# Kernel tuning notes

Measured on AMD Instinct MI355X. Metric: run time of the kernel, lower is better.

## Reference

```python
import jax, jax.numpy as jnp
import numpy as np

N_FEATURES = 16
N_FREQUENCIES = 256
TIME_AXIS = 1


def setup_inputs() -> dict:
    key = jax.random.key(0)
    x = jax.random.normal(key, (32, 4096, 16), dtype=jnp.float32)
    return {"x": x}


def reference(x):
    # x: (B, T, F)
    B, T, F = x.shape
    n = 2 * T                 # FFT length >= 2T-1 -> linear cross-correlation
    L = (T - 1) // 2          # torch 'same' left padding for kernel size T

    # rfft of zero-padded signals along time: (B, n//2+1, F)
    Xf = jnp.fft.rfft(x, n=n, axis=1)

    # Pairwise cross-spectra. Pair (i, j) corresponds to conv1d(f_i, kernel=f_j):
    #   corr_ij[t] = sum_k f_i[t + k - L] * f_j[k]  ==  irfft(Xf_i * conj(Xf_j)) shifted by L.
    P = jnp.einsum('bti,btj->btij', Xf, jnp.conj(Xf))      # (B, n//2+1, F, F)
    P = P.reshape(B, Xf.shape[1], F * F)                   # pair order = i*F + j (loop order)

    corr_full = jnp.fft.irfft(P, n=n, axis=1)              # (B, n, F*F) circular xcorr
    idx = (jnp.arange(T) - L) % n                          # 'same'-padding window of lags
    convs = corr_full[:, idx, :]                           # (B, T, F*F)

    convs_fft = jnp.fft.rfft(convs, axis=TIME_AXIS, norm='ortho')[:, :N_FREQUENCIES, :]
    return convs_fft.mean(axis=-1, keepdims=True)          # (B, n_frequencies, 1) complex64
```

## Files before the change

### kernel.cpp

```cpp
#include <hip/hip_runtime.h>
#include <hip/hip_bf16.h>


#define B_DIM 32
#define T_DIM 4096
#define NLAG 2049
#define NCHUNK 16
#define TS (T_DIM / NCHUNK)
#define PSTRIDE 2052
#define THETA 1.5339807878856412e-03f

#define SW(l) ((l) + (((l) >> 5) << 2))
#define LS_PHYS 4616

__global__ __launch_bounds__(256) void ksum(const float* __restrict__ x,
                                            float* __restrict__ s) {
    int i = blockIdx.x * 256 + threadIdx.x;
    const float4* xv = (const float4*)(x + (size_t)i * 16);
    float4 a = xv[0], b = xv[1], c = xv[2], d = xv[3];
    s[i] = ((a.x + a.y) + (a.z + a.w)) + ((b.x + b.y) + (b.z + b.w)) +
           ((c.x + c.y) + (c.z + c.w)) + ((d.x + d.y) + (d.z + d.w));
}

__global__ __launch_bounds__(256) void kautoc(const float* __restrict__ s,
                                              float* __restrict__ part) {
    __shared__ __align__(16) float ls[LS_PHYS];
    int b = blockIdx.x;
    int q = blockIdx.y;
    const float4* sb4 = (const float4*)(s + (size_t)b * T_DIM);
    for (int idx = threadIdx.x; idx < 1026; idx += 256) {
        int l = idx * 4;
        float4 v = make_float4(0.f, 0.f, 0.f, 0.f);
        if (l < T_DIM) v = sb4[idx];
        *(float4*)&ls[SW(l)] = v;
    }
    __syncthreads();

    float* pr = part + ((size_t)b * NCHUNK + q) * PSTRIDE;

    int tau0 = threadIdx.x * 8;
    int t0 = q * TS;
    int tmax = T_DIM - tau0;
    if (tmax > t0 + TS) tmax = t0 + TS;

    float acc[8] = {0.f, 0.f, 0.f, 0.f, 0.f, 0.f, 0.f, 0.f};
    if (t0 < tmax) {
        float w[16];
        {
            int l0 = t0 + tau0;
            float4 w0 = *(const float4*)&ls[SW(l0)];
            float4 w1 = *(const float4*)&ls[SW(l0 + 4)];
            w[0] = w0.x; w[1] = w0.y; w[2] = w0.z; w[3] = w0.w;
            w[4] = w1.x; w[5] = w1.y; w[6] = w1.z; w[7] = w1.w;
        }
        for (int t = t0; t + 8 <= tmax; t += 8) {
            int ln = t + tau0 + 8;
            float4 n0 = *(const float4*)&ls[SW(ln)];
            float4 n1 = *(const float4*)&ls[SW(ln + 4)];
            w[8] = n0.x;  w[9] = n0.y;  w[10] = n0.z; w[11] = n0.w;
            w[12] = n1.x; w[13] = n1.y; w[14] = n1.z; w[15] = n1.w;
            float4 a0 = *(const float4*)&ls[SW(t)];
            float4 a1 = *(const float4*)&ls[SW(t + 4)];
            float as[8] = {a0.x, a0.y, a0.z, a0.w, a1.x, a1.y, a1.z, a1.w};
            #pragma unroll
            for (int s2 = 0; s2 < 8; ++s2) {
                #pragma unroll
                for (int u = 0; u < 8; ++u)
                    acc[u] = fmaf(as[s2], w[s2 + u], acc[u]);
            }
            #pragma unroll
            for (int k = 0; k < 8; ++k) w[k] = w[k + 8];
        }
    }
    *(float4*)&pr[tau0]     = make_float4(acc[0], acc[1], acc[2], acc[3]);
    *(float4*)&pr[tau0 + 4] = make_float4(acc[4], acc[5], acc[6], acc[7]);

    if (threadIdx.x >= 192) {
        float a2 = 0.f;
        if (t0 < 2048) {
            int tend = t0 + TS;
            if (tend > 2048) tend = 2048;
            for (int t = t0 + (threadIdx.x - 192); t < tend; t += 64)
                a2 += ls[SW(t)] * ls[SW(t + 2048)];
        }
        for (int off = 32; off; off >>= 1) a2 += __shfl_down(a2, off, 64);
        if (threadIdx.x == 192) pr[2048] = a2;
    }
}

__global__ __launch_bounds__(256) void kreduce(const float* __restrict__ part,
                                               float* __restrict__ r) {
    int b = blockIdx.x;
    const float* pb = part + (size_t)b * NCHUNK * PSTRIDE;
    for (int idx = threadIdx.x; idx < 512; idx += 256) {
        float4 acc = make_float4(0.f, 0.f, 0.f, 0.f);
        #pragma unroll
        for (int q = 0; q < NCHUNK; ++q) {
            float4 v = *(const float4*)&pb[(size_t)q * PSTRIDE + idx * 4];
            acc.x += v.x; acc.y += v.y; acc.z += v.z; acc.w += v.w;
        }
        *(float4*)&r[(size_t)b * NLAG + idx * 4] = acc;
    }
    if (threadIdx.x == 0) {
        float acc = 0.f;
        #pragma unroll
        for (int q = 0; q < NCHUNK; ++q)
            acc += pb[(size_t)q * PSTRIDE + 2048];
        r[(size_t)b * NLAG + 2048] = acc;
    }
}

__global__ __launch_bounds__(256) void kdft(const float* __restrict__ r,
                                            float* __restrict__ out) {
    __shared__ float lr[NLAG];
    int b = blockIdx.x;
    const float* rb = r + (size_t)b * NLAG;
    for (int i = threadIdx.x; i < NLAG; i += 256)
        lr[i] = rb[i];
    __syncthreads();

    int m = blockIdx.y * 16 + (threadIdx.x >> 4);
    int slice = threadIdx.x & 15;
    float part = 0.0f;
    #pragma unroll 8
    for (int k = 0; k < 128; ++k) {
        int j = slice + (k << 4);
        int p = (m * j) & 4095;
        part = fmaf(lr[j], __cosf((float)p * THETA), part);
    }
    #pragma unroll
    for (int off = 8; off; off >>= 1) part += __shfl_down(part, off, 16);
    if (slice == 0) {
        float A = 2.0f * part - lr[0] + ((m & 1) ? -lr[2048] : lr[2048]);
        int qp = (2047 * m) & 4095;
        float ang = (float)qp * THETA;
        float g = A * (1.0f / 16384.0f);
        out[(size_t)b * 256 + m] = g * __cosf(ang);
        out[8192 + (size_t)b * 256 + m] = -g * __sinf(ang);
    }
}

extern "C" void kernel_launch(void* const* d_in, const int* in_sizes, int n_in,
                              void* d_out, int out_size, void* d_ws, size_t ws_size,
                              hipStream_t stream) {
    const float* x = (const float*)d_in[0];
    float* out = (float*)d_out;
    float* s = (float*)d_ws;
    float* r = s + B_DIM * T_DIM;
    float* part = r + B_DIM * NLAG;
    ksum<<<dim3(512), dim3(256), 0, stream>>>(x, s);
    kautoc<<<dim3(B_DIM, NCHUNK), dim3(256), 0, stream>>>(s, part);
    kreduce<<<dim3(B_DIM), dim3(256), 0, stream>>>(part, r);
    kdft<<<dim3(B_DIM, 16), dim3(256), 0, stream>>>(r, out);
}
```

Before: 84.07 us.

## Fuse partial reduction into DFT kernel and window autocorrelation LDS loads

Each autocorrelation block now loads only the slice of the summed signal it needs into shared memory, shrinking LDS use and making every chunk's loop bounds uniform (out-of-range samples read as zero). The separate reduction kernel is removed; the DFT kernel sums the chunk partials directly into shared memory, dropping a launch and a global round trip. The DFT grid is halved with more work per thread, at the cost of each block redundantly reducing the partials.

```diff
diff --git a/kernel.cpp b/kernel.cpp
--- a/kernel.cpp
+++ b/kernel.cpp
@@ -7,11 +7,12 @@
 #define NLAG 2049
 #define NCHUNK 16
 #define TS (T_DIM / NCHUNK)
+#define LOGI 2304
 #define PSTRIDE 2052
 #define THETA 1.5339807878856412e-03f
 
 #define SW(l) ((l) + (((l) >> 5) << 2))
-#define LS_PHYS 4616
+#define LS_PHYS 2592
 
 __global__ __launch_bounds__(256) void ksum(const float* __restrict__ x,
                                             float* __restrict__ s) {
@@ -27,69 +28,64 @@
     __shared__ __align__(16) float ls[LS_PHYS];
     int b = blockIdx.x;
     int q = blockIdx.y;
-    const float4* sb4 = (const float4*)(s + (size_t)b * T_DIM);
-    for (int idx = threadIdx.x; idx < 1026; idx += 256) {
+    int t0 = q * TS;
+    const float* sb = s + (size_t)b * T_DIM;
+    for (int idx = threadIdx.x; idx < LOGI / 4; idx += 256) {
         int l = idx * 4;
+        int g = t0 + l;
         float4 v = make_float4(0.f, 0.f, 0.f, 0.f);
-        if (l < T_DIM) v = sb4[idx];
+        if (g < T_DIM) v = *(const float4*)&sb[g];
         *(float4*)&ls[SW(l)] = v;
     }
     __syncthreads();
 
     float* pr = part + ((size_t)b * NCHUNK + q) * PSTRIDE;
-
     int tau0 = threadIdx.x * 8;
-    int t0 = q * TS;
-    int tmax = T_DIM - tau0;
-    if (tmax > t0 + TS) tmax = t0 + TS;
 
     float acc[8] = {0.f, 0.f, 0.f, 0.f, 0.f, 0.f, 0.f, 0.f};
-    if (t0 < tmax) {
-        float w[16];
-        {
-            int l0 = t0 + tau0;
-            float4 w0 = *(const float4*)&ls[SW(l0)];
-            float4 w1 = *(const float4*)&ls[SW(l0 + 4)];
-            w[0] = w0.x; w[1] = w0.y; w[2] = w0.z; w[3] = w0.w;
-            w[4] = w1.x; w[5] = w1.y; w[6] = w1.z; w[7] = w1.w;
+    float w[16];
+    {
+        float4 w0 = *(const float4*)&ls[SW(tau0)];
+        float4 w1 = *(const float4*)&ls[SW(tau0 + 4)];
+        w[0] = w0.x; w[1] = w0.y; w[2] = w0.z; w[3] = w0.w;
+        w[4] = w1.x; w[5] = w1.y; w[6] = w1.z; w[7] = w1.w;
+    }
+    #pragma unroll 4
+    for (int t = 0; t < TS; t += 8) {
+        int ln = t + tau0 + 8;
+        float4 n0 = *(const float4*)&ls[SW(ln)];
+        float4 n1 = *(const float4*)&ls[SW(ln + 4)];
+        w[8] = n0.x;  w[9] = n0.y;  w[10] = n0.z; w[11] = n0.w;
+        w[12] = n1.x; w[13] = n1.y; w[14] = n1.z; w[15] = n1.w;
+        float4 a0 = *(const float4*)&ls[SW(t)];
+        float4 a1 = *(const float4*)&ls[SW(t + 4)];
+        float as[8] = {a0.x, a0.y, a0.z, a0.w, a1.x, a1.y, a1.z, a1.w};
+        #pragma unroll
+        for (int s2 = 0; s2 < 8; ++s2) {
+            #pragma unroll
+            for (int u = 0; u < 8; ++u)
+                acc[u] = fmaf(as[s2], w[s2 + u], acc[u]);
         }
-        for (int t = t0; t + 8 <= tmax; t += 8) {
-            int ln = t + tau0 + 8;
-            float4 n0 = *(const float4*)&ls[SW(ln)];
-            float4 n1 = *(const float4*)&ls[SW(ln + 4)];
-            w[8] = n0.x;  w[9] = n0.y;  w[10] = n0.z; w[11] = n0.w;
-            w[12] = n1.x; w[13] = n1.y; w[14] = n1.z; w[15] = n1.w;
-            float4 a0 = *(const float4*)&ls[SW(t)];
-            float4 a1 = *(const float4*)&ls[SW(t + 4)];
-            float as[8] = {a0.x, a0.y, a0.z, a0.w, a1.x, a1.y, a1.z, a1.w};
-            #pragma unroll
-            for (int s2 = 0; s2 < 8; ++s2) {
-                #pragma unroll
-                for (int u = 0; u < 8; ++u)
-                    acc[u] = fmaf(as[s2], w[s2 + u], acc[u]);
-            }
-            #pragma unroll
-            for (int k = 0; k < 8; ++k) w[k] = w[k + 8];
-        }
+        #pragma unroll
+        for (int k = 0; k < 8; ++k) w[k] = w[k + 8];
     }
     *(float4*)&pr[tau0]     = make_float4(acc[0], acc[1], acc[2], acc[3]);
     *(float4*)&pr[tau0 + 4] = make_float4(acc[4], acc[5], acc[6], acc[7]);
 
     if (threadIdx.x >= 192) {
+        int sl = threadIdx.x - 192;
         float a2 = 0.f;
-        if (t0 < 2048) {
-            int tend = t0 + TS;
-            if (tend > 2048) tend = 2048;
-            for (int t = t0 + (threadIdx.x - 192); t < tend; t += 64)
-                a2 += ls[SW(t)] * ls[SW(t + 2048)];
-        }
+        #pragma unroll
+        for (int t = 0; t < TS; t += 64)
+            a2 += ls[SW(t + sl)] * ls[SW(t + sl + 2048)];
         for (int off = 32; off; off >>= 1) a2 += __shfl_down(a2, off, 64);
         if (threadIdx.x == 192) pr[2048] = a2;
     }
 }
 
-__global__ __launch_bounds__(256) void kreduce(const float* __restrict__ part,
-                                               float* __restrict__ r) {
+__global__ __launch_bounds__(256) void kdft(const float* __restrict__ part,
+                                            float* __restrict__ out) {
+    __shared__ float lr[NLAG];
     int b = blockIdx.x;
     const float* pb = part + (size_t)b * NCHUNK * PSTRIDE;
     for (int idx = threadIdx.x; idx < 512; idx += 256) {
@@ -99,39 +95,30 @@
             float4 v = *(const float4*)&pb[(size_t)q * PSTRIDE + idx * 4];
             acc.x += v.x; acc.y += v.y; acc.z += v.z; acc.w += v.w;
         }
-        *(float4*)&r[(size_t)b * NLAG + idx * 4] = acc;
+        *(float4*)&lr[idx * 4] = acc;
     }
     if (threadIdx.x == 0) {
         float acc = 0.f;
         #pragma unroll
         for (int q = 0; q < NCHUNK; ++q)
             acc += pb[(size_t)q * PSTRIDE + 2048];
-        r[(size_t)b * NLAG + 2048] = acc;
+        lr[2048] = acc;
     }
-}
-
-__global__ __launch_bounds__(256) void kdft(const float* __restrict__ r,
-                                            float* __restrict__ out) {
-    __shared__ float lr[NLAG];
-    int b = blockIdx.x;
-    const float* rb = r + (size_t)b * NLAG;
-    for (int i = threadIdx.x; i < NLAG; i += 256)
-        lr[i] = rb[i];
     __syncthreads();
 
-    int m = blockIdx.y * 16 + (threadIdx.x >> 4);
-    int slice = threadIdx.x & 15;
-    float part = 0.0f;
+    int m = blockIdx.y * 32 + (threadIdx.x >> 3);
+    int slice = threadIdx.x & 7;
+    float partsum = 0.0f;
     #pragma unroll 8
-    for (int k = 0; k < 128; ++k) {
-        int j = slice + (k << 4);
+    for (int k = 0; k < 256; ++k) {
+        int j = slice + (k << 3);
         int p = (m * j) & 4095;
-        part = fmaf(lr[j], __cosf((float)p * THETA), part);
+        partsum = fmaf(lr[j], __cosf((float)p * THETA), partsum);
     }
     #pragma unroll
-    for (int off = 8; off; off >>= 1) part += __shfl_down(part, off, 16);
+    for (int off = 4; off; off >>= 1) partsum += __shfl_down(partsum, off, 8);
     if (slice == 0) {
-        float A = 2.0f * part - lr[0] + ((m & 1) ? -lr[2048] : lr[2048]);
+        float A = 2.0f * partsum - lr[0] + ((m & 1) ? -lr[2048] : lr[2048]);
         int qp = (2047 * m) & 4095;
         float ang = (float)qp * THETA;
         float g = A * (1.0f / 16384.0f);
@@ -146,10 +133,8 @@
     const float* x = (const float*)d_in[0];
     float* out = (float*)d_out;
     float* s = (float*)d_ws;
-    float* r = s + B_DIM * T_DIM;
-    float* part = r + B_DIM * NLAG;
+    float* part = s + B_DIM * T_DIM;
     ksum<<<dim3(512), dim3(256), 0, stream>>>(x, s);
     kautoc<<<dim3(B_DIM, NCHUNK), dim3(256), 0, stream>>>(s, part);
-    kreduce<<<dim3(B_DIM), dim3(256), 0, stream>>>(part, r);
-    kdft<<<dim3(B_DIM, 16), dim3(256), 0, stream>>>(r, out);
+    kdft<<<dim3(B_DIM, 8), dim3(256), 0, stream>>>(part, out);
 }
```

Measured after the change: 79.12 us. -5.9%, faster.
